# Kernel optimization log

Measured on AMD Instinct MI355X. Metric: run time of the kernel, lower is better.

The kernel has to match this reference:

```python
import jax, jax.numpy as jnp
import numpy as np

EPS = 1e-5
PI = 3.1415927410125732
B, C, N = 32, 3, 4096


def setup_inputs() -> dict:
    key = jax.random.key(0)
    ks = jax.random.split(key, 16)
    rn = lambda k, shape, scale: (jax.random.normal(k, shape, jnp.float32) * scale)
    z = lambda n: jnp.zeros((n,), jnp.float32)
    o = lambda n: jnp.ones((n,), jnp.float32)
    return {
        "x": jax.random.normal(ks[0], (B, C, N), jnp.float32),
        # conv1x1 weights stored as [out, in] (Conv1d kernel size 1)
        "w1": rn(ks[1], (64, C), 0.5), "b1": z(64), "g1": o(64), "be1": z(64),
        "w2": rn(ks[2], (128, 64), 0.12), "b2": z(128), "g2": o(128), "be2": z(128),
        "w3": rn(ks[3], (1024, 128), 0.09), "b3": z(1024), "g3": o(1024), "be3": z(1024),
        "fw1": rn(ks[4], (512, 1024), 0.03), "fb1": z(512), "g4": o(512), "be4": z(512),
        "fw2": rn(ks[5], (256, 512), 0.044), "fb2": z(256), "g5": o(256), "be5": z(256),
        "fw3": rn(ks[6], (128, 256), 0.0625), "fb3": z(128), "g6": o(128), "be6": z(128),
        "fw4": rn(ks[7], (3, 128), 0.088), "fb4": z(3),
    }


def _bn_cn(h, g, b):
    # BatchNorm1d on [B, C, N]: stats over (batch, spatial), biased variance (train mode)
    m = h.mean((0, 2), keepdims=True)
    v = ((h - m) ** 2).mean((0, 2), keepdims=True)
    return g[None, :, None] * (h - m) * jax.lax.rsqrt(v + EPS) + b[None, :, None]


def _bn_fc(h, g, b):
    # BatchNorm1d on [B, C]: stats over batch
    m = h.mean(0, keepdims=True)
    v = ((h - m) ** 2).mean(0, keepdims=True)
    return g * (h - m) * jax.lax.rsqrt(v + EPS) + b


def _euler_to_rot(ang):
    # ang: [B, 3] = (rx, ry, rz);  R = Rz @ Ry @ Rx per sample
    a, b, c = ang[:, 0], ang[:, 1], ang[:, 2]
    ca, sa = jnp.cos(a), jnp.sin(a)
    cb, sb = jnp.cos(b), jnp.sin(b)
    cc, sc = jnp.cos(c), jnp.sin(c)
    one = jnp.ones_like(a); zero = jnp.zeros_like(a)
    Rx = jnp.stack([jnp.stack([one, zero, zero], -1),
                    jnp.stack([zero, ca, -sa], -1),
                    jnp.stack([zero, sa, ca], -1)], -2)
    Ry = jnp.stack([jnp.stack([cb, zero, sb], -1),
                    jnp.stack([zero, one, zero], -1),
                    jnp.stack([-sb, zero, cb], -1)], -2)
    Rz = jnp.stack([jnp.stack([cc, -sc, zero], -1),
                    jnp.stack([sc, cc, zero], -1),
                    jnp.stack([zero, zero, one], -1)], -2)
    return jnp.matmul(Rz, jnp.matmul(Ry, Rx))  # [B, 3, 3]


def reference(x, w1, b1, g1, be1, w2, b2, g2, be2, w3, b3, g3, be3,
              fw1, fb1, g4, be4, fw2, fb2, g5, be5, fw3, fb3, g6, be6, fw4, fb4):
    h = jax.nn.relu(_bn_cn(jnp.einsum('bcn,oc->bon', x, w1) + b1[None, :, None], g1, be1))
    h = jax.nn.relu(_bn_cn(jnp.einsum('bcn,oc->bon', h, w2) + b2[None, :, None], g2, be2))
    h = jax.nn.relu(_bn_cn(jnp.einsum('bcn,oc->bon', h, w3) + b3[None, :, None], g3, be3))
    h = h.max(axis=2)  # global max pool -> [B, 1024]
    h = jax.nn.relu(_bn_fc(h @ fw1.T + fb1, g4, be4))
    h = jax.nn.relu(_bn_fc(h @ fw2.T + fb2, g5, be5))
    h = jax.nn.relu(_bn_fc(h @ fw3.T + fb3, g6, be6))
    ang = (h @ fw4.T + fb4) * PI  # [B, 3] Euler angles
    return _euler_to_rot(ang)
```

## Files before the change

kernel.cpp:

```cpp
#include <hip/hip_runtime.h>
#include <math.h>


#define EPS 1e-5f
#define PI_F 3.1415927410125732f

typedef unsigned int u32;
typedef unsigned short u16;
typedef __bf16 bf16x8 __attribute__((ext_vector_type(8)));
typedef float f32x4 __attribute__((ext_vector_type(4)));

#define AS1 __attribute__((address_space(1)))
#define AS3 __attribute__((address_space(3)))

__device__ __forceinline__ u16 f2bf(float f) {
  u32 u = __float_as_uint(f);
  return (u16)((u + 0x7FFFu + ((u >> 16) & 1u)) >> 16);
}
__device__ __forceinline__ float bf2f(u16 h) { return __uint_as_float(((u32)h) << 16); }

__global__ __launch_bounds__(256) void kA_xpart(const float* __restrict__ x,
    float* __restrict__ xst_part) {
  __shared__ float wsum[4][9];
  int t = threadIdx.x;
  int tg = blockIdx.x * 256 + t;
  int b = tg >> 10, nq = (tg & 1023) << 2;
  const float* xb = x + ((size_t)b * 3) * 4096 + nq;
  float4 a = *(const float4*)(xb);
  float4 c = *(const float4*)(xb + 4096);
  float4 d = *(const float4*)(xb + 8192);
  float p[9];
  p[0] = (a.x + a.y) + (a.z + a.w);
  p[1] = (c.x + c.y) + (c.z + c.w);
  p[2] = (d.x + d.y) + (d.z + d.w);
  p[3] = fmaf(a.x,a.x, fmaf(a.y,a.y, fmaf(a.z,a.z, a.w*a.w)));
  p[4] = fmaf(a.x,c.x, fmaf(a.y,c.y, fmaf(a.z,c.z, a.w*c.w)));
  p[5] = fmaf(a.x,d.x, fmaf(a.y,d.y, fmaf(a.z,d.z, a.w*d.w)));
  p[6] = fmaf(c.x,c.x, fmaf(c.y,c.y, fmaf(c.z,c.z, c.w*c.w)));
  p[7] = fmaf(c.x,d.x, fmaf(c.y,d.y, fmaf(c.z,d.z, c.w*d.w)));
  p[8] = fmaf(d.x,d.x, fmaf(d.y,d.y, fmaf(d.z,d.z, d.w*d.w)));
  #pragma unroll
  for (int k = 0; k < 9; ++k) {
    #pragma unroll
    for (int s = 1; s < 64; s <<= 1) p[k] += __shfl_xor(p[k], s);
  }
  if ((t & 63) == 0) {
    #pragma unroll
    for (int k = 0; k < 9; ++k) wsum[t >> 6][k] = p[k];
  }
  __syncthreads();
  if (t < 9) xst_part[blockIdx.x*9 + t] = wsum[0][t] + wsum[1][t] + wsum[2][t] + wsum[3][t];
}

__global__ __launch_bounds__(256) void kC2_gram(const float* __restrict__ x,
    const float* __restrict__ xst_part,
    const float* __restrict__ w1, const float* __restrict__ b1,
    const float* __restrict__ g1, const float* __restrict__ be1,
    float* __restrict__ gram_part, float* __restrict__ w1f_g, float* __restrict__ b1f_g) {
  __shared__ float xsl[3][1024];
  __shared__ float4 w1s4[64];
  __shared__ __align__(16) char hfrag[4352];
  __shared__ __align__(16) char lfrag[4352];
  __shared__ float mred[256];
  __shared__ float xstL[9];
  int t = threadIdx.x, bi = blockIdx.x;
  int lane = t & 63, wid = t >> 6;
  if (t < 9) { float s = 0.f; for (int p = 0; p < 128; ++p) s += xst_part[p*9 + t]; xstL[t] = s; }
  int b = bi >> 2, n0 = (bi & 3) << 10;
  for (int i = t; i < 3072; i += 256) {
    int c = i >> 10, n = i & 1023;
    xsl[c][n] = x[((size_t)b*3 + c)*4096 + n0 + n];
  }
  __syncthreads();
  if (t < 64) {
    const float inv = 1.f/131072.f;
    float mx = xstL[0]*inv, my = xstL[1]*inv, mz = xstL[2]*inv;
    float cxx = xstL[3]*inv - mx*mx, cxy = xstL[4]*inv - mx*my, cxz = xstL[5]*inv - mx*mz;
    float cyy = xstL[6]*inv - my*my, cyz = xstL[7]*inv - my*mz, czz = xstL[8]*inv - mz*mz;
    float wa = w1[t*3], wb = w1[t*3+1], wc = w1[t*3+2];
    float mu = fmaf(wa, mx, fmaf(wb, my, fmaf(wc, mz, b1[t])));
    float var = wa*wa*cxx + wb*wb*cyy + wc*wc*czz
              + 2.f*(wa*wb*cxy + wa*wc*cxz + wb*wc*cyz);
    float s = g1[t] * rsqrtf(var + EPS);
    float bf = be1[t] + s*(b1[t] - mu);
    w1s4[t] = make_float4(s*wa, s*wb, s*wc, bf);
    if (bi == 0) { w1f_g[t*3] = s*wa; w1f_g[t*3+1] = s*wb; w1f_g[t*3+2] = s*wc; b1f_g[t] = bf; }
  }
  __syncthreads();
  int ch = t & 63, ptg = t >> 6;
  float4 wv = w1s4[ch];
  int wbyte = (ch >> 4)*1088 + (((ch & 15) | (ptg << 4)) << 4);
  const f32x4 zero4 = {0.f,0.f,0.f,0.f};
  f32x4 acc[4] = {zero4, zero4, zero4, zero4};
  float msum = 0.f;
  for (int it = 0; it < 32; ++it) {
    int p0 = (it << 5) | (ptg << 3);
    u32 hw[4], lw[4];
    #pragma unroll
    for (int q = 0; q < 4; ++q) {
      int pA = p0 + 2*q, pB = p0 + 2*q + 1;
      float v0 = fmaxf(fmaf(wv.x, xsl[0][pA], fmaf(wv.y, xsl[1][pA], fmaf(wv.z, xsl[2][pA], wv.w))), 0.f);
      float v1 = fmaxf(fmaf(wv.x, xsl[0][pB], fmaf(wv.y, xsl[1][pB], fmaf(wv.z, xsl[2][pB], wv.w))), 0.f);
      msum += v0 + v1;
      u16 h0 = f2bf(v0), h1 = f2bf(v1);
      hw[q] = (u32)h0 | ((u32)h1 << 16);
      lw[q] = (u32)f2bf(v0 - bf2f(h0)) | ((u32)f2bf(v1 - bf2f(h1)) << 16);
    }
    *(uint4*)(hfrag + wbyte) = make_uint4(hw[0],hw[1],hw[2],hw[3]);
    *(uint4*)(lfrag + wbyte) = make_uint4(lw[0],lw[1],lw[2],lw[3]);
    __syncthreads();
    bf16x8 ah = *(const bf16x8*)(hfrag + wid*1088 + (lane << 4));
    bf16x8 al = *(const bf16x8*)(lfrag + wid*1088 + (lane << 4));
    #pragma unroll
    for (int cg = 0; cg < 4; ++cg) {
      bf16x8 bh = *(const bf16x8*)(hfrag + cg*1088 + (lane << 4));
      bf16x8 bl = *(const bf16x8*)(lfrag + cg*1088 + (lane << 4));
      acc[cg] = __builtin_amdgcn_mfma_f32_16x16x32_bf16(al, bh, acc[cg], 0, 0, 0);
      acc[cg] = __builtin_amdgcn_mfma_f32_16x16x32_bf16(ah, bl, acc[cg], 0, 0, 0);
      acc[cg] = __builtin_amdgcn_mfma_f32_16x16x32_bf16(ah, bh, acc[cg], 0, 0, 0);
    }
    __syncthreads();
  }
  mred[t] = msum;
  __syncthreads();
  if (t < 64)
    gram_part[(size_t)bi*4160 + 4096 + t] = mred[t] + mred[t+64] + mred[t+128] + mred[t+192];
  #pragma unroll
  for (int cg = 0; cg < 4; ++cg) {
    #pragma unroll
    for (int r = 0; r < 4; ++r) {
      int i = (wid << 4) | (((lane >> 4) << 2) | r);
      int j = (cg << 4) | (lane & 15);
      gram_part[(size_t)bi*4160 + i*64 + j] = acc[cg][r];
    }
  }
}

__global__ __launch_bounds__(256) void kR_gramred(const float* __restrict__ gram_part,
    float* __restrict__ gram) {
  int cell = blockIdx.x * 256 + threadIdx.x;
  if (cell >= 4160) return;
  float s = 0.f;
  for (int blk = 0; blk < 128; ++blk) s += gram_part[(size_t)blk*4160 + cell];
  gram[cell] = s;
}

__global__ __launch_bounds__(64) void kD_fold2(const float* __restrict__ gram,
    const float* __restrict__ w2, const float* __restrict__ b2,
    const float* __restrict__ g2, const float* __restrict__ be2,
    float* __restrict__ w2f, float* __restrict__ b2f) {
  __shared__ float wrow[64];
  int o = blockIdx.x, i = threadIdx.x;
  wrow[i] = w2[o*64 + i];
  __syncthreads();
  float si = 0.f;
  #pragma unroll 8
  for (int j = 0; j < 64; ++j) si = fmaf(wrow[j], gram[j*64 + i], si);
  const float inv = 1.f / 131072.f;
  float qi = wrow[i] * si;
  float di = wrow[i] * (gram[4096 + i] * inv);
  #pragma unroll
  for (int d2 = 1; d2 < 64; d2 <<= 1) { qi += __shfl_xor(qi, d2); di += __shfl_xor(di, d2); }
  float mu2 = di + b2[o];
  float var = qi*inv - di*di;
  float s = g2[o] * rsqrtf(var + EPS);
  w2f[o*64 + i] = s * wrow[i];
  if (i == 0) b2f[o] = be2[o] + s*(b2[o] - mu2);
}

__global__ __launch_bounds__(256) void kE2_layer2(const float* __restrict__ x,
    const float* __restrict__ w1f, const float* __restrict__ b1f,
    const float* __restrict__ w2f, const float* __restrict__ b2f,
    u16* __restrict__ h2t_hi, u16* __restrict__ h2t_lo) {
  __shared__ float xs[3][256];
  __shared__ float4 w1s4[64];
  __shared__ __align__(16) char h1h[17408];
  __shared__ __align__(16) char h1l[17408];
  int t = threadIdx.x;
  int b = ((blockIdx.x & 7) << 2) | ((blockIdx.x >> 3) & 3);
  int ntile = (blockIdx.x >> 5) << 8;
  int lane = t & 63, wid = t >> 6;
  int wo = wid & 1, wn = wid >> 1;
  #pragma unroll
  for (int i = 0; i < 3; ++i) {
    int idx = (i << 8) | t;
    int c = idx >> 8, n = idx & 255;
    xs[c][n] = x[((size_t)b*3 + c)*4096 + ntile + n];
  }
  if (t < 64) w1s4[t] = make_float4(w1f[t*3], w1f[t*3+1], w1f[t*3+2], b1f[t]);
  bf16x8 wf_hi[4][2], wf_lo[4][2];
  float4 bvv[4];
  #pragma unroll
  for (int of = 0; of < 4; ++of) {
    int o2r = (wo << 6) | (of << 4) | (lane & 15);
    bvv[of] = *(const float4*)(b2f + (wo << 6) + (of << 4) + ((lane >> 4) << 2));
    #pragma unroll
    for (int ks1 = 0; ks1 < 2; ++ks1) {
      const float* src = w2f + o2r*64 + (ks1 << 5) + ((lane >> 4) << 3);
      float4 f0 = *(const float4*)src;
      float4 f1 = *(const float4*)(src + 4);
      float fv[8] = {f0.x,f0.y,f0.z,f0.w, f1.x,f1.y,f1.z,f1.w};
      u32 hw[4], lw[4];
      #pragma unroll
      for (int p2 = 0; p2 < 4; ++p2) {
        u16 h0 = f2bf(fv[2*p2]), h1 = f2bf(fv[2*p2+1]);
        u16 l0 = f2bf(fv[2*p2] - bf2f(h0)), l1 = f2bf(fv[2*p2+1] - bf2f(h1));
        hw[p2] = (u32)h0 | ((u32)h1 << 16);
        lw[p2] = (u32)l0 | ((u32)l1 << 16);
      }
      uint4 H = make_uint4(hw[0],hw[1],hw[2],hw[3]);
      uint4 L = make_uint4(lw[0],lw[1],lw[2],lw[3]);
      wf_hi[of][ks1] = *(const bf16x8*)&H;
      wf_lo[of][ks1] = *(const bf16x8*)&L;
    }
  }
  __syncthreads();
  const f32x4 zero4 = {0.f,0.f,0.f,0.f};
  for (int chunk = 0; chunk < 2; ++chunk) {
    {
      int n = t >> 1, ks1 = t & 1;
      int nL = (chunk << 7) | n;
      float xa = xs[0][nL], xb = xs[1][nL], xc = xs[2][nL];
      int fb = (((n >> 4) << 1) | ks1) * 1088 + ((n & 15) << 4);
      #pragma unroll
      for (int kq = 0; kq < 4; ++kq) {
        u32 hw[4], lw[4];
        #pragma unroll
        for (int p2 = 0; p2 < 4; ++p2) {
          int k1 = (ks1 << 5) | (kq << 3) | (p2 << 1);
          float4 wv0 = w1s4[k1];
          float4 wv1 = w1s4[k1 + 1];
          float v0 = fmaxf(fmaf(wv0.x, xa, fmaf(wv0.y, xb, fmaf(wv0.z, xc, wv0.w))), 0.f);
          float v1 = fmaxf(fmaf(wv1.x, xa, fmaf(wv1.y, xb, fmaf(wv1.z, xc, wv1.w))), 0.f);
          u16 h0 = f2bf(v0), h1_ = f2bf(v1);
          hw[p2] = (u32)h0 | ((u32)h1_ << 16);
          lw[p2] = (u32)f2bf(v0 - bf2f(h0)) | ((u32)f2bf(v1 - bf2f(h1_)) << 16);
        }
        *(uint4*)(h1h + fb + (kq << 8)) = make_uint4(hw[0],hw[1],hw[2],hw[3]);
        *(uint4*)(h1l + fb + (kq << 8)) = make_uint4(lw[0],lw[1],lw[2],lw[3]);
      }
    }
    __syncthreads();
    #pragma unroll
    for (int nb = 0; nb < 4; ++nb) {
      int fbase = (((wn << 2) | nb) << 1) * 1088 + (lane << 4);
      bf16x8 bh0 = *(const bf16x8*)(h1h + fbase);
      bf16x8 bh1 = *(const bf16x8*)(h1h + fbase + 1088);
      bf16x8 bl0 = *(const bf16x8*)(h1l + fbase);
      bf16x8 bl1 = *(const bf16x8*)(h1l + fbase + 1088);
      int nblk_g = (ntile >> 4) | (chunk << 3) | (wn << 2) | nb;
      #pragma unroll
      for (int of = 0; of < 4; ++of) {
        f32x4 acc;
        acc = __builtin_amdgcn_mfma_f32_16x16x32_bf16(wf_hi[of][0], bl0, zero4, 0, 0, 0);
        acc = __builtin_amdgcn_mfma_f32_16x16x32_bf16(wf_lo[of][0], bh0, acc, 0, 0, 0);
        acc = __builtin_amdgcn_mfma_f32_16x16x32_bf16(wf_hi[of][0], bh0, acc, 0, 0, 0);
        acc = __builtin_amdgcn_mfma_f32_16x16x32_bf16(wf_hi[of][1], bl1, acc, 0, 0, 0);
        acc = __builtin_amdgcn_mfma_f32_16x16x32_bf16(wf_lo[of][1], bh1, acc, 0, 0, 0);
        acc = __builtin_amdgcn_mfma_f32_16x16x32_bf16(wf_hi[of][1], bh1, acc, 0, 0, 0);
        ushort4 hs, ls;
        float v0 = fmaxf(acc[0] + bvv[of].x, 0.f);
        float v1 = fmaxf(acc[1] + bvv[of].y, 0.f);
        float v2 = fmaxf(acc[2] + bvv[of].z, 0.f);
        float v3 = fmaxf(acc[3] + bvv[of].w, 0.f);
        hs.x = f2bf(v0); hs.y = f2bf(v1); hs.z = f2bf(v2); hs.w = f2bf(v3);
        ls.x = f2bf(v0 - bf2f(hs.x)); ls.y = f2bf(v1 - bf2f(hs.y));
        ls.z = f2bf(v2 - bf2f(hs.z)); ls.w = f2bf(v3 - bf2f(hs.w));
        int ks2 = (wo << 1) | (of >> 1);
        int q = ((of & 1) << 1) | ((lane >> 5) & 1);
        int l = (lane & 15) | (q << 4);
        int j0 = ((lane >> 4) & 1) << 2;
        size_t idx = ((((size_t)((b << 8) | nblk_g) << 2) | ks2) << 9) + (l << 3) + j0;
        *(ushort4*)(h2t_hi + idx) = hs;
        *(ushort4*)(h2t_lo + idx) = ls;
      }
    }
    __syncthreads();
  }
}

__global__ __launch_bounds__(256, 2) void k5_layer3(
    const u16* __restrict__ h2t_hi, const u16* __restrict__ h2t_lo,
    const float* __restrict__ w3,
    float* __restrict__ sum3, float* __restrict__ sq3,
    float* __restrict__ maxv, float* __restrict__ minv) {
  __shared__ __align__(16) char smem[65536];
  const int t = threadIdx.x, lane = t & 63, wid = t >> 6;
  const int g = blockIdx.x & 63, otile = blockIdx.x >> 6;
  const int b = g >> 1, half = g & 1;

  const size_t gbase = ((size_t)b << 19) | ((size_t)half << 18);
  auto STAGE = [&](int c, int buf) {
    char* lb = smem + (buf << 15);
    size_t gb = gbase + ((size_t)c << 13);
    #pragma unroll
    for (int i = 0; i < 4; ++i) {
      int off = (i << 12) | (t << 4);
      __builtin_amdgcn_global_load_lds((const AS1 u32*)(h2t_hi + gb + (off >> 1)),
          (AS3 u32*)(lb + off), 16, 0, 0);
    }
    #pragma unroll
    for (int i = 0; i < 4; ++i) {
      int off = (i << 12) | (t << 4);
      __builtin_amdgcn_global_load_lds((const AS1 u32*)(h2t_lo + gb + (off >> 1)),
          (AS3 u32*)(lb + 16384 + off), 16, 0, 0);
    }
  };
  STAGE(0, 0); STAGE(1, 1);

  bf16x8 wh[4][4], wl[4][4];
  #pragma unroll
  for (int of = 0; of < 4; ++of) {
    int o3 = (otile << 6) | (of << 4) | (lane & 15);
    #pragma unroll
    for (int ks = 0; ks < 4; ++ks) {
      const float* src = w3 + (size_t)o3*128 + (ks << 5) + ((lane >> 4) << 3);
      float4 f0 = *(const float4*)src;
      float4 f1 = *(const float4*)(src + 4);
      float fv[8] = {f0.x,f0.y,f0.z,f0.w, f1.x,f1.y,f1.z,f1.w};
      u32 hw[4], lw[4];
      #pragma unroll
      for (int p2 = 0; p2 < 4; ++p2) {
        u16 h0 = f2bf(fv[2*p2]), h1 = f2bf(fv[2*p2+1]);
        u16 l0 = f2bf(fv[2*p2] - bf2f(h0)), l1 = f2bf(fv[2*p2+1] - bf2f(h1));
        hw[p2] = (u32)h0 | ((u32)h1 << 16);
        lw[p2] = (u32)l0 | ((u32)l1 << 16);
      }
      uint4 H = make_uint4(hw[0],hw[1],hw[2],hw[3]);
      uint4 L = make_uint4(lw[0],lw[1],lw[2],lw[3]);
      wh[ks][of] = *(const bf16x8*)&H;
      wl[ks][of] = *(const bf16x8*)&L;
    }
  }

  const f32x4 zero4 = {0.f,0.f,0.f,0.f};
  f32x4 acc[4];
  float rs[4] = {0.f,0.f,0.f,0.f};
  float rq[4] = {0.f,0.f,0.f,0.f};
  float rmx[4] = {-3.4e38f,-3.4e38f,-3.4e38f,-3.4e38f};
  float rmn[4] = { 3.4e38f, 3.4e38f, 3.4e38f, 3.4e38f};

  for (int c = 0; c < 32; ++c) {
    if (c < 31) asm volatile("s_waitcnt vmcnt(8)" ::: "memory");
    else        asm volatile("s_waitcnt vmcnt(0)" ::: "memory");
    __builtin_amdgcn_s_barrier();
    const char* bb = smem + ((c & 1) << 15) + (wid << 12) + (lane << 4);
    __builtin_amdgcn_s_setprio(1);
    #pragma unroll
    for (int ks = 0; ks < 4; ++ks) {
      bf16x8 ah = *(const bf16x8*)(bb + (ks << 10));
      bf16x8 al = *(const bf16x8*)(bb + 16384 + (ks << 10));
      #pragma unroll
      for (int of = 0; of < 4; ++of) {
        f32x4 c0 = ks ? acc[of] : zero4;
        c0 = __builtin_amdgcn_mfma_f32_16x16x32_bf16(al, wh[ks][of], c0, 0, 0, 0);
        c0 = __builtin_amdgcn_mfma_f32_16x16x32_bf16(ah, wl[ks][of], c0, 0, 0, 0);
        acc[of] = __builtin_amdgcn_mfma_f32_16x16x32_bf16(ah, wh[ks][of], c0, 0, 0, 0);
      }
    }
    __builtin_amdgcn_s_setprio(0);
    #pragma unroll
    for (int of = 0; of < 4; ++of) {
      f32x4 v = acc[of];
      rs[of] += (v[0] + v[1]) + (v[2] + v[3]);
      rq[of] = fmaf(v[0],v[0], fmaf(v[1],v[1], fmaf(v[2],v[2], fmaf(v[3],v[3], rq[of]))));
      rmx[of] = fmaxf(rmx[of], fmaxf(fmaxf(v[0],v[1]), fmaxf(v[2],v[3])));
      rmn[of] = fminf(rmn[of], fminf(fminf(v[0],v[1]), fminf(v[2],v[3])));
    }
    __builtin_amdgcn_s_barrier();
    if (c < 30) STAGE(c + 2, c & 1);
  }

  #pragma unroll
  for (int of = 0; of < 4; ++of) {
    rs[of] += __shfl_xor(rs[of], 16); rs[of] += __shfl_xor(rs[of], 32);
    rq[of] += __shfl_xor(rq[of], 16); rq[of] += __shfl_xor(rq[of], 32);
    rmx[of] = fmaxf(rmx[of], __shfl_xor(rmx[of], 16)); rmx[of] = fmaxf(rmx[of], __shfl_xor(rmx[of], 32));
    rmn[of] = fminf(rmn[of], __shfl_xor(rmn[of], 16)); rmn[of] = fminf(rmn[of], __shfl_xor(rmn[of], 32));
  }
  __syncthreads();
  float* part = (float*)smem;
  if (lane < 16) {
    #pragma unroll
    for (int of = 0; of < 4; ++of) {
      float* pp = part + ((((wid << 2) | of) << 4) + lane) * 4;
      pp[0] = rs[of]; pp[1] = rq[of]; pp[2] = rmx[of]; pp[3] = rmn[of];
    }
  }
  __syncthreads();
  if (t < 64) {
    int of = t >> 4, ol = t & 15;
    float S = 0.f, Q = 0.f, MX = -3.4e38f, MN = 3.4e38f;
    #pragma unroll
    for (int wn = 0; wn < 4; ++wn) {
      const float* pp = part + ((((wn << 2) | of) << 4) + ol) * 4;
      S += pp[0]; Q += pp[1]; MX = fmaxf(MX, pp[2]); MN = fminf(MN, pp[3]);
    }
    int go = (((half << 5) | b) << 10) | (otile << 6) | t;
    sum3[go] = S; sq3[go] = Q; maxv[go] = MX; minv[go] = MN;
  }
}

__global__ void k_fin3_pool(const float* __restrict__ sum3, const float* __restrict__ sq3,
    const float* __restrict__ maxv, const float* __restrict__ minv,
    const float* __restrict__ b3,
    const float* __restrict__ g, const float* __restrict__ be, float* __restrict__ pool) {
  int o = blockIdx.x*256 + threadIdx.x;
  float S = 0.f, Q = 0.f;
  for (int h = 0; h < 2; ++h)
    for (int b = 0; b < 32; ++b) { int gi = (((h<<5)|b)<<10) | o; S += sum3[gi]; Q += sq3[gi]; }
  const float inv = 1.f/131072.f;
  float ma = S*inv;
  float m = ma + b3[o];
  float var = Q*inv - ma*ma;
  float sc = g[o]*rsqrtf(var + EPS);
  float sh = be[o] - sc*m;
  bool pos = (sc >= 0.f);
  for (int b = 0; b < 32; ++b) {
    int g0 = (b << 10) | o, g1 = ((32 + b) << 10) | o;
    float v = pos ? fmaxf(maxv[g0], maxv[g1]) : fminf(minv[g0], minv[g1]);
    pool[(b << 10) | o] = fmaxf(fmaf(sc, v + b3[o], sh), 0.f);
  }
}

__global__ __launch_bounds__(256) void k_fc_bn_relu(const float* __restrict__ in,
    const float* __restrict__ w, const float* __restrict__ fb,
    const float* __restrict__ g, const float* __restrict__ be,
    float* __restrict__ out, int K, int F) {
  __shared__ float wrow[1024];
  __shared__ float preb[32];
  int o = blockIdx.x, t = threadIdx.x;
  for (int k = t; k < K; k += 256) wrow[k] = w[(size_t)o*K + k];
  __syncthreads();
  int b = t >> 3, j = t & 7;
  int per = K >> 3;
  const float* inb = in + (size_t)b*K + j*per;
  const float* wp  = wrow + j*per;
  float p = 0.f;
  for (int k = 0; k < per; ++k) p = fmaf(inb[k], wp[k], p);
  p += __shfl_xor(p, 1); p += __shfl_xor(p, 2); p += __shfl_xor(p, 4);
  if (j == 0) preb[b] = p + fb[o];
  __syncthreads();
  if (t < 32) {
    float v = preb[t];
    float s = v;
    #pragma unroll
    for (int d = 1; d < 32; d <<= 1) s += __shfl_xor(s, d);
    float m = s * 0.03125f;
    float dv = v - m;
    float q = dv*dv;
    #pragma unroll
    for (int d = 1; d < 32; d <<= 1) q += __shfl_xor(q, d);
    float var = q * 0.03125f;
    float sc = g[o]*rsqrtf(var + EPS);
    out[(size_t)t*F + o] = fmaxf(fmaf(sc, dv, be[o]), 0.f);
  }
}

__global__ __launch_bounds__(128) void k_final(const float* __restrict__ h6,
    const float* __restrict__ fw4, const float* __restrict__ fb4, float* __restrict__ out) {
  __shared__ float angs[32][3];
  int t = threadIdx.x;
  if (t < 96) {
    int b = t / 3, j = t % 3;
    float p = 0.f;
    #pragma unroll 4
    for (int k = 0; k < 128; ++k) p = fmaf(h6[b*128+k], fw4[j*128+k], p);
    angs[b][j] = (p + fb4[j]) * PI_F;
  }
  __syncthreads();
  if (t < 32) {
    float a = angs[t][0], bb = angs[t][1], c = angs[t][2];
    float sa, ca; sincosf(a,  &sa, &ca);
    float sb, cb; sincosf(bb, &sb, &cb);
    float sc, cc; sincosf(c,  &sc, &cc);
    float* o9 = out + t*9;
    o9[0] = cc*cb;
    o9[1] = fmaf(cc*sb, sa, -sc*ca);
    o9[2] = fmaf(cc*sb, ca,  sc*sa);
    o9[3] = sc*cb;
    o9[4] = fmaf(sc*sb, sa,  cc*ca);
    o9[5] = fmaf(sc*sb, ca, -cc*sa);
    o9[6] = -sb;
    o9[7] = cb*sa;
    o9[8] = cb*ca;
  }
}

extern "C" void kernel_launch(void* const* d_in, const int* in_sizes, int n_in,
                              void* d_out, int out_size, void* d_ws, size_t ws_size,
                              hipStream_t stream) {
  (void)in_sizes; (void)n_in; (void)out_size; (void)ws_size;
  const float* x   = (const float*)d_in[0];
  const float* w1  = (const float*)d_in[1];
  const float* b1  = (const float*)d_in[2];
  const float* g1  = (const float*)d_in[3];
  const float* be1 = (const float*)d_in[4];
  const float* w2  = (const float*)d_in[5];
  const float* b2  = (const float*)d_in[6];
  const float* g2  = (const float*)d_in[7];
  const float* be2 = (const float*)d_in[8];
  const float* w3  = (const float*)d_in[9];
  const float* b3  = (const float*)d_in[10];
  const float* g3  = (const float*)d_in[11];
  const float* be3 = (const float*)d_in[12];
  const float* fw1 = (const float*)d_in[13];
  const float* fb1 = (const float*)d_in[14];
  const float* g4  = (const float*)d_in[15];
  const float* be4 = (const float*)d_in[16];
  const float* fw2 = (const float*)d_in[17];
  const float* fb2 = (const float*)d_in[18];
  const float* g5p = (const float*)d_in[19];
  const float* be5 = (const float*)d_in[20];
  const float* fw3 = (const float*)d_in[21];
  const float* fb3 = (const float*)d_in[22];
  const float* g6  = (const float*)d_in[23];
  const float* be6 = (const float*)d_in[24];
  const float* fw4 = (const float*)d_in[25];
  const float* fb4 = (const float*)d_in[26];

  u16* h2t_hi = (u16*)d_ws;
  u16* h2t_lo = (u16*)d_ws + 16777216;
  float* gram_part = (float*)d_ws;
  float* acc0 = (float*)d_ws + 16777216;
  float* xst_part = acc0;
  float* w1f  = acc0 + 1152;
  float* b1f  = acc0 + 1344;
  float* w2f  = acc0 + 1408;
  float* b2f  = acc0 + 9600;
  float* gram = acc0 + 9728;
  float* sum3 = acc0 + 13888;
  float* sq3  = acc0 + 79424;
  float* maxv = acc0 + 144960;
  float* minv = acc0 + 210496;
  float* pool = acc0 + 276032;
  float* h4v  = acc0 + 308800;
  float* h5v  = acc0 + 325184;
  float* h6v  = acc0 + 333376;

  kA_xpart<<<128, 256, 0, stream>>>(x, xst_part);
  kC2_gram<<<128, 256, 0, stream>>>(x, xst_part, w1, b1, g1, be1, gram_part, w1f, b1f);
  kR_gramred<<<17, 256, 0, stream>>>(gram_part, gram);
  kD_fold2<<<128, 64, 0, stream>>>(gram, w2, b2, g2, be2, w2f, b2f);
  kE2_layer2<<<512, 256, 0, stream>>>(x, w1f, b1f, w2f, b2f, h2t_hi, h2t_lo);
  k5_layer3<<<1024, 256, 0, stream>>>(h2t_hi, h2t_lo, w3, sum3, sq3, maxv, minv);
  k_fin3_pool<<<4, 256, 0, stream>>>(sum3, sq3, maxv, minv, b3, g3, be3, pool);
  k_fc_bn_relu<<<512, 256, 0, stream>>>(pool, fw1, fb1, g4, be4, h4v, 1024, 512);
  k_fc_bn_relu<<<256, 256, 0, stream>>>(h4v, fw2, fb2, g5p, be5, h5v, 512, 256);
  k_fc_bn_relu<<<128, 256, 0, stream>>>(h5v, fw3, fb3, g6, be6, h6v, 256, 128);
  k_final<<<1, 128, 0, stream>>>(h6v, fw4, fb4, (float*)d_out);
}
```

Before: 200.4 us.

## Fuse pooling, FC tail and rotation into one cooperative kernel with grid syncs

```diff
diff --git a/kernel.cpp b/kernel.cpp
--- a/kernel.cpp
+++ b/kernel.cpp
@@ -1,9 +1,12 @@
 #include <hip/hip_runtime.h>
+#include <hip/hip_cooperative_groups.h>
 #include <math.h>
 
 
 #define EPS 1e-5f
 #define PI_F 3.1415927410125732f
+
+namespace cg = cooperative_groups;
 
 typedef unsigned int u32;
 typedef unsigned short u16;
@@ -112,12 +115,12 @@
     bf16x8 ah = *(const bf16x8*)(hfrag + wid*1088 + (lane << 4));
     bf16x8 al = *(const bf16x8*)(lfrag + wid*1088 + (lane << 4));
     #pragma unroll
-    for (int cg = 0; cg < 4; ++cg) {
-      bf16x8 bh = *(const bf16x8*)(hfrag + cg*1088 + (lane << 4));
-      bf16x8 bl = *(const bf16x8*)(lfrag + cg*1088 + (lane << 4));
-      acc[cg] = __builtin_amdgcn_mfma_f32_16x16x32_bf16(al, bh, acc[cg], 0, 0, 0);
-      acc[cg] = __builtin_amdgcn_mfma_f32_16x16x32_bf16(ah, bl, acc[cg], 0, 0, 0);
-      acc[cg] = __builtin_amdgcn_mfma_f32_16x16x32_bf16(ah, bh, acc[cg], 0, 0, 0);
+    for (int cg2 = 0; cg2 < 4; ++cg2) {
+      bf16x8 bh = *(const bf16x8*)(hfrag + cg2*1088 + (lane << 4));
+      bf16x8 bl = *(const bf16x8*)(lfrag + cg2*1088 + (lane << 4));
+      acc[cg2] = __builtin_amdgcn_mfma_f32_16x16x32_bf16(al, bh, acc[cg2], 0, 0, 0);
+      acc[cg2] = __builtin_amdgcn_mfma_f32_16x16x32_bf16(ah, bl, acc[cg2], 0, 0, 0);
+      acc[cg2] = __builtin_amdgcn_mfma_f32_16x16x32_bf16(ah, bh, acc[cg2], 0, 0, 0);
     }
     __syncthreads();
   }
@@ -126,12 +129,12 @@
   if (t < 64)
     gram_part[(size_t)bi*4160 + 4096 + t] = mred[t] + mred[t+64] + mred[t+128] + mred[t+192];
   #pragma unroll
-  for (int cg = 0; cg < 4; ++cg) {
+  for (int cg2 = 0; cg2 < 4; ++cg2) {
     #pragma unroll
     for (int r = 0; r < 4; ++r) {
       int i = (wid << 4) | (((lane >> 4) << 2) | r);
-      int j = (cg << 4) | (lane & 15);
-      gram_part[(size_t)bi*4160 + i*64 + j] = acc[cg][r];
+      int j = (cg2 << 4) | (lane & 15);
+      gram_part[(size_t)bi*4160 + i*64 + j] = acc[cg2][r];
     }
   }
 }
@@ -345,17 +348,21 @@
     else        asm volatile("s_waitcnt vmcnt(0)" ::: "memory");
     __builtin_amdgcn_s_barrier();
     const char* bb = smem + ((c & 1) << 15) + (wid << 12) + (lane << 4);
+    bf16x8 ah[4], al[4];
+    #pragma unroll
+    for (int ks = 0; ks < 4; ++ks) {
+      ah[ks] = *(const bf16x8*)(bb + (ks << 10));
+      al[ks] = *(const bf16x8*)(bb + 16384 + (ks << 10));
+    }
     __builtin_amdgcn_s_setprio(1);
     #pragma unroll
     for (int ks = 0; ks < 4; ++ks) {
-      bf16x8 ah = *(const bf16x8*)(bb + (ks << 10));
-      bf16x8 al = *(const bf16x8*)(bb + 16384 + (ks << 10));
       #pragma unroll
       for (int of = 0; of < 4; ++of) {
         f32x4 c0 = ks ? acc[of] : zero4;
-        c0 = __builtin_amdgcn_mfma_f32_16x16x32_bf16(al, wh[ks][of], c0, 0, 0, 0);
-        c0 = __builtin_amdgcn_mfma_f32_16x16x32_bf16(ah, wl[ks][of], c0, 0, 0, 0);
-        acc[of] = __builtin_amdgcn_mfma_f32_16x16x32_bf16(ah, wh[ks][of], c0, 0, 0, 0);
+        c0 = __builtin_amdgcn_mfma_f32_16x16x32_bf16(al[ks], wh[ks][of], c0, 0, 0, 0);
+        c0 = __builtin_amdgcn_mfma_f32_16x16x32_bf16(ah[ks], wl[ks][of], c0, 0, 0, 0);
+        acc[of] = __builtin_amdgcn_mfma_f32_16x16x32_bf16(ah[ks], wh[ks][of], c0, 0, 0, 0);
       }
     }
     __builtin_amdgcn_s_setprio(0);
@@ -364,8 +371,8 @@
       f32x4 v = acc[of];
       rs[of] += (v[0] + v[1]) + (v[2] + v[3]);
       rq[of] = fmaf(v[0],v[0], fmaf(v[1],v[1], fmaf(v[2],v[2], fmaf(v[3],v[3], rq[of]))));
-      rmx[of] = fmaxf(rmx[of], fmaxf(fmaxf(v[0],v[1]), fmaxf(v[2],v[3])));
-      rmn[of] = fminf(rmn[of], fminf(fminf(v[0],v[1]), fminf(v[2],v[3])));
+      rmx[of] = fmaxf(fmaxf(rmx[of], fmaxf(v[0],v[1])), fmaxf(v[2],v[3]));
+      rmn[of] = fminf(fminf(rmn[of], fminf(v[0],v[1])), fminf(v[2],v[3]));
     }
     __builtin_amdgcn_s_barrier();
     if (c < 30) STAGE(c + 2, c & 1);
@@ -401,35 +408,10 @@
   }
 }
 
-__global__ void k_fin3_pool(const float* __restrict__ sum3, const float* __restrict__ sq3,
-    const float* __restrict__ maxv, const float* __restrict__ minv,
-    const float* __restrict__ b3,
-    const float* __restrict__ g, const float* __restrict__ be, float* __restrict__ pool) {
-  int o = blockIdx.x*256 + threadIdx.x;
-  float S = 0.f, Q = 0.f;
-  for (int h = 0; h < 2; ++h)
-    for (int b = 0; b < 32; ++b) { int gi = (((h<<5)|b)<<10) | o; S += sum3[gi]; Q += sq3[gi]; }
-  const float inv = 1.f/131072.f;
-  float ma = S*inv;
-  float m = ma + b3[o];
-  float var = Q*inv - ma*ma;
-  float sc = g[o]*rsqrtf(var + EPS);
-  float sh = be[o] - sc*m;
-  bool pos = (sc >= 0.f);
-  for (int b = 0; b < 32; ++b) {
-    int g0 = (b << 10) | o, g1 = ((32 + b) << 10) | o;
-    float v = pos ? fmaxf(maxv[g0], maxv[g1]) : fminf(minv[g0], minv[g1]);
-    pool[(b << 10) | o] = fmaxf(fmaf(sc, v + b3[o], sh), 0.f);
-  }
-}
-
-__global__ __launch_bounds__(256) void k_fc_bn_relu(const float* __restrict__ in,
+__device__ __forceinline__ void fc_one(int o, const float* __restrict__ in,
     const float* __restrict__ w, const float* __restrict__ fb,
     const float* __restrict__ g, const float* __restrict__ be,
-    float* __restrict__ out, int K, int F) {
-  __shared__ float wrow[1024];
-  __shared__ float preb[32];
-  int o = blockIdx.x, t = threadIdx.x;
+    float* __restrict__ out, int K, int F, float* wrow, float* preb, int t) {
   for (int k = t; k < K; k += 256) wrow[k] = w[(size_t)o*K + k];
   __syncthreads();
   int b = t >> 3, j = t & 7;
@@ -455,35 +437,80 @@
     float sc = g[o]*rsqrtf(var + EPS);
     out[(size_t)t*F + o] = fmaxf(fmaf(sc, dv, be[o]), 0.f);
   }
-}
-
-__global__ __launch_bounds__(128) void k_final(const float* __restrict__ h6,
-    const float* __restrict__ fw4, const float* __restrict__ fb4, float* __restrict__ out) {
+  __syncthreads();
+}
+
+__global__ __launch_bounds__(256) void k_tail(
+    const float* __restrict__ sum3, const float* __restrict__ sq3,
+    const float* __restrict__ maxv, const float* __restrict__ minv,
+    const float* __restrict__ b3, const float* __restrict__ g3, const float* __restrict__ be3,
+    const float* __restrict__ fw1, const float* __restrict__ fb1,
+    const float* __restrict__ g4, const float* __restrict__ be4,
+    const float* __restrict__ fw2, const float* __restrict__ fb2,
+    const float* __restrict__ g5, const float* __restrict__ be5,
+    const float* __restrict__ fw3, const float* __restrict__ fb3,
+    const float* __restrict__ g6, const float* __restrict__ be6,
+    const float* __restrict__ fw4, const float* __restrict__ fb4,
+    float* __restrict__ pool, float* __restrict__ h4v,
+    float* __restrict__ h5v, float* __restrict__ h6v,
+    float* __restrict__ out) {
+  cg::grid_group grid = cg::this_grid();
+  __shared__ float wrow[1024];
+  __shared__ float preb[32];
   __shared__ float angs[32][3];
-  int t = threadIdx.x;
-  if (t < 96) {
-    int b = t / 3, j = t % 3;
-    float p = 0.f;
-    #pragma unroll 4
-    for (int k = 0; k < 128; ++k) p = fmaf(h6[b*128+k], fw4[j*128+k], p);
-    angs[b][j] = (p + fb4[j]) * PI_F;
-  }
-  __syncthreads();
-  if (t < 32) {
-    float a = angs[t][0], bb = angs[t][1], c = angs[t][2];
-    float sa, ca; sincosf(a,  &sa, &ca);
-    float sb, cb; sincosf(bb, &sb, &cb);
-    float sc, cc; sincosf(c,  &sc, &cc);
-    float* o9 = out + t*9;
-    o9[0] = cc*cb;
-    o9[1] = fmaf(cc*sb, sa, -sc*ca);
-    o9[2] = fmaf(cc*sb, ca,  sc*sa);
-    o9[3] = sc*cb;
-    o9[4] = fmaf(sc*sb, sa,  cc*ca);
-    o9[5] = fmaf(sc*sb, ca, -cc*sa);
-    o9[6] = -sb;
-    o9[7] = cb*sa;
-    o9[8] = cb*ca;
+  int t = threadIdx.x, bi = blockIdx.x;
+  {
+    int o = (bi << 2) | (t >> 6);
+    int l = t & 63;
+    int gi = (l << 10) | o;
+    float S = sum3[gi], Q = sq3[gi];
+    #pragma unroll
+    for (int d = 1; d < 64; d <<= 1) { S += __shfl_xor(S, d); Q += __shfl_xor(Q, d); }
+    const float inv = 1.f/131072.f;
+    float ma = S*inv;
+    float m = ma + b3[o];
+    float var = Q*inv - ma*ma;
+    float sc = g3[o]*rsqrtf(var + EPS);
+    float sh = be3[o] - sc*m;
+    if (l < 32) {
+      int g0 = (l << 10) | o, g1 = ((32 + l) << 10) | o;
+      float v = (sc >= 0.f) ? fmaxf(maxv[g0], maxv[g1]) : fminf(minv[g0], minv[g1]);
+      pool[(l << 10) | o] = fmaxf(fmaf(sc, v + b3[o], sh), 0.f);
+    }
+  }
+  grid.sync();
+  fc_one(bi*2,     pool, fw1, fb1, g4, be4, h4v, 1024, 512, wrow, preb, t);
+  fc_one(bi*2 + 1, pool, fw1, fb1, g4, be4, h4v, 1024, 512, wrow, preb, t);
+  grid.sync();
+  fc_one(bi, h4v, fw2, fb2, g5, be5, h5v, 512, 256, wrow, preb, t);
+  grid.sync();
+  if (bi < 128) fc_one(bi, h5v, fw3, fb3, g6, be6, h6v, 256, 128, wrow, preb, t);
+  grid.sync();
+  if (bi == 0) {
+    if (t < 96) {
+      int b = t / 3, j = t % 3;
+      float p = 0.f;
+      #pragma unroll 4
+      for (int k = 0; k < 128; ++k) p = fmaf(h6v[b*128 + k], fw4[j*128 + k], p);
+      angs[b][j] = (p + fb4[j]) * PI_F;
+    }
+    __syncthreads();
+    if (t < 32) {
+      float a = angs[t][0], bb = angs[t][1], c = angs[t][2];
+      float sa, ca; sincosf(a,  &sa, &ca);
+      float sb, cb; sincosf(bb, &sb, &cb);
+      float sc, cc; sincosf(c,  &sc, &cc);
+      float* o9 = out + t*9;
+      o9[0] = cc*cb;
+      o9[1] = fmaf(cc*sb, sa, -sc*ca);
+      o9[2] = fmaf(cc*sb, ca,  sc*sa);
+      o9[3] = sc*cb;
+      o9[4] = fmaf(sc*sb, sa,  cc*ca);
+      o9[5] = fmaf(sc*sb, ca, -cc*sa);
+      o9[6] = -sb;
+      o9[7] = cb*sa;
+      o9[8] = cb*ca;
+    }
   }
 }
 
@@ -544,9 +571,15 @@
   kD_fold2<<<128, 64, 0, stream>>>(gram, w2, b2, g2, be2, w2f, b2f);
   kE2_layer2<<<512, 256, 0, stream>>>(x, w1f, b1f, w2f, b2f, h2t_hi, h2t_lo);
   k5_layer3<<<1024, 256, 0, stream>>>(h2t_hi, h2t_lo, w3, sum3, sq3, maxv, minv);
-  k_fin3_pool<<<4, 256, 0, stream>>>(sum3, sq3, maxv, minv, b3, g3, be3, pool);
-  k_fc_bn_relu<<<512, 256, 0, stream>>>(pool, fw1, fb1, g4, be4, h4v, 1024, 512);
-  k_fc_bn_relu<<<256, 256, 0, stream>>>(h4v, fw2, fb2, g5p, be5, h5v, 512, 256);
-  k_fc_bn_relu<<<128, 256, 0, stream>>>(h5v, fw3, fb3, g6, be6, h6v, 256, 128);
-  k_final<<<1, 128, 0, stream>>>(h6v, fw4, fb4, (float*)d_out);
-}
+
+  float* outp = (float*)d_out;
+  void* args[] = { (void*)&sum3, (void*)&sq3, (void*)&maxv, (void*)&minv,
+                   (void*)&b3, (void*)&g3, (void*)&be3,
+                   (void*)&fw1, (void*)&fb1, (void*)&g4, (void*)&be4,
+                   (void*)&fw2, (void*)&fb2, (void*)&g5p, (void*)&be5,
+                   (void*)&fw3, (void*)&fb3, (void*)&g6, (void*)&be6,
+                   (void*)&fw4, (void*)&fb4,
+                   (void*)&pool, (void*)&h4v, (void*)&h5v, (void*)&h6v,
+                   (void*)&outp };
+  hipLaunchCooperativeKernel((void*)k_tail, dim3(256), dim3(256), args, 0, stream);
+}
```

Result: slower. 312.3 us (+55.8%).

## Retile layer3 GEMM with triple buffering, XCD-aware mapping and atomic stat reduction

Applied to the files above, without the earlier changes.

```diff
diff --git a/kernel.cpp b/kernel.cpp
--- a/kernel.cpp
+++ b/kernel.cpp
@@ -18,6 +18,13 @@
   return (u16)((u + 0x7FFFu + ((u >> 16) & 1u)) >> 16);
 }
 __device__ __forceinline__ float bf2f(u16 h) { return __uint_as_float(((u32)h) << 16); }
+__device__ __forceinline__ u32 encf(float f) {
+  u32 u = __float_as_uint(f);
+  return (u & 0x80000000u) ? ~u : (u | 0x80000000u);
+}
+__device__ __forceinline__ float decf(u32 u) {
+  return __uint_as_float((u & 0x80000000u) ? (u ^ 0x80000000u) : ~u);
+}
 
 __global__ __launch_bounds__(256) void kA_xpart(const float* __restrict__ x,
     float* __restrict__ xst_part) {
@@ -112,12 +119,12 @@
     bf16x8 ah = *(const bf16x8*)(hfrag + wid*1088 + (lane << 4));
     bf16x8 al = *(const bf16x8*)(lfrag + wid*1088 + (lane << 4));
     #pragma unroll
-    for (int cg = 0; cg < 4; ++cg) {
-      bf16x8 bh = *(const bf16x8*)(hfrag + cg*1088 + (lane << 4));
-      bf16x8 bl = *(const bf16x8*)(lfrag + cg*1088 + (lane << 4));
-      acc[cg] = __builtin_amdgcn_mfma_f32_16x16x32_bf16(al, bh, acc[cg], 0, 0, 0);
-      acc[cg] = __builtin_amdgcn_mfma_f32_16x16x32_bf16(ah, bl, acc[cg], 0, 0, 0);
-      acc[cg] = __builtin_amdgcn_mfma_f32_16x16x32_bf16(ah, bh, acc[cg], 0, 0, 0);
+    for (int cg2 = 0; cg2 < 4; ++cg2) {
+      bf16x8 bh = *(const bf16x8*)(hfrag + cg2*1088 + (lane << 4));
+      bf16x8 bl = *(const bf16x8*)(lfrag + cg2*1088 + (lane << 4));
+      acc[cg2] = __builtin_amdgcn_mfma_f32_16x16x32_bf16(al, bh, acc[cg2], 0, 0, 0);
+      acc[cg2] = __builtin_amdgcn_mfma_f32_16x16x32_bf16(ah, bl, acc[cg2], 0, 0, 0);
+      acc[cg2] = __builtin_amdgcn_mfma_f32_16x16x32_bf16(ah, bh, acc[cg2], 0, 0, 0);
     }
     __syncthreads();
   }
@@ -126,12 +133,12 @@
   if (t < 64)
     gram_part[(size_t)bi*4160 + 4096 + t] = mred[t] + mred[t+64] + mred[t+128] + mred[t+192];
   #pragma unroll
-  for (int cg = 0; cg < 4; ++cg) {
+  for (int cg2 = 0; cg2 < 4; ++cg2) {
     #pragma unroll
     for (int r = 0; r < 4; ++r) {
       int i = (wid << 4) | (((lane >> 4) << 2) | r);
-      int j = (cg << 4) | (lane & 15);
-      gram_part[(size_t)bi*4160 + i*64 + j] = acc[cg][r];
+      int j = (cg2 << 4) | (lane & 15);
+      gram_part[(size_t)bi*4160 + i*64 + j] = acc[cg2][r];
     }
   }
 }
@@ -279,39 +286,42 @@
   }
 }
 
-__global__ __launch_bounds__(256, 2) void k5_layer3(
+__global__ __launch_bounds__(256, 3) void k5_layer3(
     const u16* __restrict__ h2t_hi, const u16* __restrict__ h2t_lo,
     const float* __restrict__ w3,
     float* __restrict__ sum3, float* __restrict__ sq3,
-    float* __restrict__ maxv, float* __restrict__ minv) {
-  __shared__ __align__(16) char smem[65536];
+    u32* __restrict__ maxe, u32* __restrict__ mine) {
+  __shared__ __align__(16) char smem[49152];
   const int t = threadIdx.x, lane = t & 63, wid = t >> 6;
-  const int g = blockIdx.x & 63, otile = blockIdx.x >> 6;
-  const int b = g >> 1, half = g & 1;
-
-  const size_t gbase = ((size_t)b << 19) | ((size_t)half << 18);
+  const int id = blockIdx.x;
+  const int xcd = id & 7, rest = id >> 3;
+  const int gq = rest & 15, otile = rest >> 4;
+  const int g = (gq << 3) | xcd;
+  const int b = g >> 2, q = g & 3;
+
+  const size_t gbase = ((size_t)((b << 8) + (q << 6))) << 11;
   auto STAGE = [&](int c, int buf) {
-    char* lb = smem + (buf << 15);
-    size_t gb = gbase + ((size_t)c << 13);
-    #pragma unroll
-    for (int i = 0; i < 4; ++i) {
+    char* lb = smem + buf * 16384;
+    size_t gb = gbase + ((size_t)c << 12);
+    #pragma unroll
+    for (int i = 0; i < 2; ++i) {
       int off = (i << 12) | (t << 4);
       __builtin_amdgcn_global_load_lds((const AS1 u32*)(h2t_hi + gb + (off >> 1)),
           (AS3 u32*)(lb + off), 16, 0, 0);
     }
     #pragma unroll
-    for (int i = 0; i < 4; ++i) {
+    for (int i = 0; i < 2; ++i) {
       int off = (i << 12) | (t << 4);
       __builtin_amdgcn_global_load_lds((const AS1 u32*)(h2t_lo + gb + (off >> 1)),
-          (AS3 u32*)(lb + 16384 + off), 16, 0, 0);
+          (AS3 u32*)(lb + 8192 + off), 16, 0, 0);
     }
   };
-  STAGE(0, 0); STAGE(1, 1);
-
-  bf16x8 wh[4][4], wl[4][4];
-  #pragma unroll
-  for (int of = 0; of < 4; ++of) {
-    int o3 = (otile << 6) | (of << 4) | (lane & 15);
+  STAGE(0, 0); STAGE(1, 1); STAGE(2, 2);
+
+  bf16x8 wh[4][2], wl[4][2];
+  #pragma unroll
+  for (int of = 0; of < 2; ++of) {
+    int o3 = (otile << 7) | (wid << 5) | (of << 4) | (lane & 15);
     #pragma unroll
     for (int ks = 0; ks < 4; ++ks) {
       const float* src = w3 + (size_t)o3*128 + (ks << 5) + ((lane >> 4) << 3);
@@ -334,81 +344,77 @@
   }
 
   const f32x4 zero4 = {0.f,0.f,0.f,0.f};
-  f32x4 acc[4];
-  float rs[4] = {0.f,0.f,0.f,0.f};
-  float rq[4] = {0.f,0.f,0.f,0.f};
-  float rmx[4] = {-3.4e38f,-3.4e38f,-3.4e38f,-3.4e38f};
-  float rmn[4] = { 3.4e38f, 3.4e38f, 3.4e38f, 3.4e38f};
+  float rs[2] = {0.f,0.f}, rq[2] = {0.f,0.f};
+  float rmx[2] = {-3.4e38f,-3.4e38f}, rmn[2] = {3.4e38f,3.4e38f};
 
   for (int c = 0; c < 32; ++c) {
-    if (c < 31) asm volatile("s_waitcnt vmcnt(8)" ::: "memory");
-    else        asm volatile("s_waitcnt vmcnt(0)" ::: "memory");
+    if (c < 30)       asm volatile("s_waitcnt vmcnt(8)" ::: "memory");
+    else if (c == 30) asm volatile("s_waitcnt vmcnt(4)" ::: "memory");
+    else              asm volatile("s_waitcnt vmcnt(0)" ::: "memory");
     __builtin_amdgcn_s_barrier();
-    const char* bb = smem + ((c & 1) << 15) + (wid << 12) + (lane << 4);
-    __builtin_amdgcn_s_setprio(1);
-    #pragma unroll
-    for (int ks = 0; ks < 4; ++ks) {
-      bf16x8 ah = *(const bf16x8*)(bb + (ks << 10));
-      bf16x8 al = *(const bf16x8*)(bb + 16384 + (ks << 10));
+    const char* bb = smem + (c % 3) * 16384 + (lane << 4);
+    #pragma unroll
+    for (int nf = 0; nf < 2; ++nf) {
+      bf16x8 ah[4], al[4];
       #pragma unroll
-      for (int of = 0; of < 4; ++of) {
-        f32x4 c0 = ks ? acc[of] : zero4;
-        c0 = __builtin_amdgcn_mfma_f32_16x16x32_bf16(al, wh[ks][of], c0, 0, 0, 0);
-        c0 = __builtin_amdgcn_mfma_f32_16x16x32_bf16(ah, wl[ks][of], c0, 0, 0, 0);
-        acc[of] = __builtin_amdgcn_mfma_f32_16x16x32_bf16(ah, wh[ks][of], c0, 0, 0, 0);
+      for (int ks = 0; ks < 4; ++ks) {
+        int fo = ((nf << 2) | ks) << 10;
+        ah[ks] = *(const bf16x8*)(bb + fo);
+        al[ks] = *(const bf16x8*)(bb + 8192 + fo);
       }
-    }
-    __builtin_amdgcn_s_setprio(0);
-    #pragma unroll
-    for (int of = 0; of < 4; ++of) {
-      f32x4 v = acc[of];
-      rs[of] += (v[0] + v[1]) + (v[2] + v[3]);
-      rq[of] = fmaf(v[0],v[0], fmaf(v[1],v[1], fmaf(v[2],v[2], fmaf(v[3],v[3], rq[of]))));
-      rmx[of] = fmaxf(rmx[of], fmaxf(fmaxf(v[0],v[1]), fmaxf(v[2],v[3])));
-      rmn[of] = fminf(rmn[of], fminf(fminf(v[0],v[1]), fminf(v[2],v[3])));
+      f32x4 a0, a1;
+      __builtin_amdgcn_s_setprio(1);
+      #pragma unroll
+      for (int ks = 0; ks < 4; ++ks) {
+        f32x4 c0 = ks ? a0 : zero4;
+        f32x4 c1 = ks ? a1 : zero4;
+        c0 = __builtin_amdgcn_mfma_f32_16x16x32_bf16(al[ks], wh[ks][0], c0, 0, 0, 0);
+        c0 = __builtin_amdgcn_mfma_f32_16x16x32_bf16(ah[ks], wl[ks][0], c0, 0, 0, 0);
+        a0 = __builtin_amdgcn_mfma_f32_16x16x32_bf16(ah[ks], wh[ks][0], c0, 0, 0, 0);
+        c1 = __builtin_amdgcn_mfma_f32_16x16x32_bf16(al[ks], wh[ks][1], c1, 0, 0, 0);
+        c1 = __builtin_amdgcn_mfma_f32_16x16x32_bf16(ah[ks], wl[ks][1], c1, 0, 0, 0);
+        a1 = __builtin_amdgcn_mfma_f32_16x16x32_bf16(ah[ks], wh[ks][1], c1, 0, 0, 0);
+      }
+      __builtin_amdgcn_s_setprio(0);
+      rs[0] += (a0[0] + a0[1]) + (a0[2] + a0[3]);
+      rq[0] = fmaf(a0[0],a0[0], fmaf(a0[1],a0[1], fmaf(a0[2],a0[2], fmaf(a0[3],a0[3], rq[0]))));
+      rmx[0] = fmaxf(fmaxf(rmx[0], fmaxf(a0[0],a0[1])), fmaxf(a0[2],a0[3]));
+      rmn[0] = fminf(fminf(rmn[0], fminf(a0[0],a0[1])), fminf(a0[2],a0[3]));
+      rs[1] += (a1[0] + a1[1]) + (a1[2] + a1[3]);
+      rq[1] = fmaf(a1[0],a1[0], fmaf(a1[1],a1[1], fmaf(a1[2],a1[2], fmaf(a1[3],a1[3], rq[1]))));
+      rmx[1] = fmaxf(fmaxf(rmx[1], fmaxf(a1[0],a1[1])), fmaxf(a1[2],a1[3]));
+      rmn[1] = fminf(fminf(rmn[1], fminf(a1[0],a1[1])), fminf(a1[2],a1[3]));
     }
     __builtin_amdgcn_s_barrier();
-    if (c < 30) STAGE(c + 2, c & 1);
-  }
-
-  #pragma unroll
-  for (int of = 0; of < 4; ++of) {
+    if (c < 29) STAGE(c + 3, (c + 3) % 3);
+  }
+
+  #pragma unroll
+  for (int of = 0; of < 2; ++of) {
     rs[of] += __shfl_xor(rs[of], 16); rs[of] += __shfl_xor(rs[of], 32);
     rq[of] += __shfl_xor(rq[of], 16); rq[of] += __shfl_xor(rq[of], 32);
     rmx[of] = fmaxf(rmx[of], __shfl_xor(rmx[of], 16)); rmx[of] = fmaxf(rmx[of], __shfl_xor(rmx[of], 32));
     rmn[of] = fminf(rmn[of], __shfl_xor(rmn[of], 16)); rmn[of] = fminf(rmn[of], __shfl_xor(rmn[of], 32));
   }
-  __syncthreads();
-  float* part = (float*)smem;
   if (lane < 16) {
     #pragma unroll
-    for (int of = 0; of < 4; ++of) {
-      float* pp = part + ((((wid << 2) | of) << 4) + lane) * 4;
-      pp[0] = rs[of]; pp[1] = rq[of]; pp[2] = rmx[of]; pp[3] = rmn[of];
-    }
-  }
-  __syncthreads();
-  if (t < 64) {
-    int of = t >> 4, ol = t & 15;
-    float S = 0.f, Q = 0.f, MX = -3.4e38f, MN = 3.4e38f;
-    #pragma unroll
-    for (int wn = 0; wn < 4; ++wn) {
-      const float* pp = part + ((((wn << 2) | of) << 4) + ol) * 4;
-      S += pp[0]; Q += pp[1]; MX = fmaxf(MX, pp[2]); MN = fminf(MN, pp[3]);
-    }
-    int go = (((half << 5) | b) << 10) | (otile << 6) | t;
-    sum3[go] = S; sq3[go] = Q; maxv[go] = MX; minv[go] = MN;
+    for (int of = 0; of < 2; ++of) {
+      int go = (b << 10) | (otile << 7) | (wid << 5) | (of << 4) | lane;
+      atomicAdd(&sum3[go], rs[of]);
+      atomicAdd(&sq3[go], rq[of]);
+      atomicMax(&maxe[go], encf(rmx[of]));
+      atomicMin(&mine[go], encf(rmn[of]));
+    }
   }
 }
 
 __global__ void k_fin3_pool(const float* __restrict__ sum3, const float* __restrict__ sq3,
-    const float* __restrict__ maxv, const float* __restrict__ minv,
+    const u32* __restrict__ maxe, const u32* __restrict__ mine,
     const float* __restrict__ b3,
     const float* __restrict__ g, const float* __restrict__ be, float* __restrict__ pool) {
   int o = blockIdx.x*256 + threadIdx.x;
   float S = 0.f, Q = 0.f;
-  for (int h = 0; h < 2; ++h)
-    for (int b = 0; b < 32; ++b) { int gi = (((h<<5)|b)<<10) | o; S += sum3[gi]; Q += sq3[gi]; }
+  for (int b = 0; b < 32; ++b) { S += sum3[(b<<10)|o]; Q += sq3[(b<<10)|o]; }
   const float inv = 1.f/131072.f;
   float ma = S*inv;
   float m = ma + b3[o];
@@ -417,9 +423,8 @@
   float sh = be[o] - sc*m;
   bool pos = (sc >= 0.f);
   for (int b = 0; b < 32; ++b) {
-    int g0 = (b << 10) | o, g1 = ((32 + b) << 10) | o;
-    float v = pos ? fmaxf(maxv[g0], maxv[g1]) : fminf(minv[g0], minv[g1]);
-    pool[(b << 10) | o] = fmaxf(fmaf(sc, v + b3[o], sh), 0.f);
+    float v = decf(pos ? maxe[(b<<10)|o] : mine[(b<<10)|o]) + b3[o];
+    pool[(b<<10)|o] = fmaxf(fmaf(sc, v, sh), 0.f);
   }
 }
 
@@ -530,21 +535,24 @@
   float* b2f  = acc0 + 9600;
   float* gram = acc0 + 9728;
   float* sum3 = acc0 + 13888;
-  float* sq3  = acc0 + 79424;
-  float* maxv = acc0 + 144960;
-  float* minv = acc0 + 210496;
-  float* pool = acc0 + 276032;
-  float* h4v  = acc0 + 308800;
-  float* h5v  = acc0 + 325184;
-  float* h6v  = acc0 + 333376;
+  float* sq3  = acc0 + 46656;
+  u32*   maxe = (u32*)(acc0 + 79424);
+  u32*   mine = (u32*)(acc0 + 112192);
+  float* pool = acc0 + 144960;
+  float* h4v  = acc0 + 177728;
+  float* h5v  = acc0 + 194112;
+  float* h6v  = acc0 + 202304;
+
+  hipMemsetAsync(acc0 + 13888, 0, 3ull*32768*4, stream);
+  hipMemsetAsync(acc0 + 112192, 0xFF, 32768ull*4, stream);
 
   kA_xpart<<<128, 256, 0, stream>>>(x, xst_part);
   kC2_gram<<<128, 256, 0, stream>>>(x, xst_part, w1, b1, g1, be1, gram_part, w1f, b1f);
   kR_gramred<<<17, 256, 0, stream>>>(gram_part, gram);
   kD_fold2<<<128, 64, 0, stream>>>(gram, w2, b2, g2, be2, w2f, b2f);
   kE2_layer2<<<512, 256, 0, stream>>>(x, w1f, b1f, w2f, b2f, h2t_hi, h2t_lo);
-  k5_layer3<<<1024, 256, 0, stream>>>(h2t_hi, h2t_lo, w3, sum3, sq3, maxv, minv);
-  k_fin3_pool<<<4, 256, 0, stream>>>(sum3, sq3, maxv, minv, b3, g3, be3, pool);
+  k5_layer3<<<1024, 256, 0, stream>>>(h2t_hi, h2t_lo, w3, sum3, sq3, maxe, mine);
+  k_fin3_pool<<<4, 256, 0, stream>>>(sum3, sq3, maxe, mine, b3, g3, be3, pool);
   k_fc_bn_relu<<<512, 256, 0, stream>>>(pool, fw1, fb1, g4, be4, h4v, 1024, 512);
   k_fc_bn_relu<<<256, 256, 0, stream>>>(h4v, fw2, fb2, g5p, be5, h5v, 512, 256);
   k_fc_bn_relu<<<128, 256, 0, stream>>>(h5v, fw3, fb3, g6, be6, h6v, 256, 128);
```

Result: faster. 192.5 us (-4.0%).
